# Kernel optimization log

Hardware: AMD Instinct MI355X
Metric: run time of the kernel (lower is better)

## Reference

```python
import jax, jax.numpy as jnp
import numpy as np

B, T, E, DH = 4, 4096, 1024, 128

def setup_inputs() -> dict:
    key = jax.random.key(0)
    k1, k2, k3, k4 = jax.random.split(key, 4)
    scale = 1.0 / np.sqrt(E)
    return {
        "norm_inputs": jax.random.normal(k1, (B, T, E), dtype=jnp.float32),
        "Wq": jax.random.normal(k2, (E, DH), dtype=jnp.float32) * scale,
        "Wk": jax.random.normal(k3, (E, DH), dtype=jnp.float32) * scale,
        "Wv": jax.random.normal(k4, (E, DH), dtype=jnp.float32) * scale,
    }

def reference(norm_inputs, Wq, Wk, Wv):
    # q,k,v: [B,T,DH]
    q = jnp.einsum("bte,ed->btd", norm_inputs, Wq)
    k = jnp.einsum("bte,ed->btd", norm_inputs, Wk)
    v = jnp.einsum("bte,ed->btd", norm_inputs, Wv)
    Tn = norm_inputs.shape[1]
    # scaled scores [B,T,T]
    scores = jnp.einsum("bqd,bkd->bqk", q, k) / jnp.sqrt(jnp.asarray(q.shape[-1], q.dtype))
    causal = jnp.tril(jnp.ones((Tn, Tn), dtype=bool))
    scores = jnp.where(causal, scores, -jnp.inf)
    attn = jax.nn.softmax(scores, axis=-1)  # dropout p=0 -> identity
    return jnp.einsum("bqk,bkd->bqd", attn, v)
```

## Files before the change

### kernel.cpp

```cpp
#include <hip/hip_runtime.h>
#include <hip/hip_bf16.h>

#define NB 4
#define NT 4096
#define NE 1024
#define ND 128
#define QSCALE 0.12751741f

typedef unsigned u32x4 __attribute__((ext_vector_type(4)));
typedef float f32x4 __attribute__((ext_vector_type(4)));
typedef float f32x16 __attribute__((ext_vector_type(16)));
typedef __bf16 bf16x8 __attribute__((ext_vector_type(8)));
typedef unsigned short u16;

__device__ __forceinline__ unsigned cvt_pk_bf16(float lo, float hi) {
  unsigned r;
  asm("v_cvt_pk_bf16_f32 %0, %1, %2" : "=v"(r) : "v"(lo), "v"(hi));
  return r;
}
__device__ __forceinline__ void permswap(unsigned& a, unsigned& b) {
  asm("v_permlane32_swap_b32 %0, %1" : "+v"(a), "+v"(b));
}
__device__ __forceinline__ u16 f2bf(float f) {
  unsigned x = __float_as_uint(f);
  x += 0x7fffu + ((x >> 16) & 1u);
  return (u16)(x >> 16);
}
__device__ __forceinline__ float bf2f(u16 u) {
  return __uint_as_float(((unsigned)u) << 16);
}
__device__ __forceinline__ f32x16 mfma32(bf16x8 a, bf16x8 b, f32x16 c) {
  return __builtin_amdgcn_mfma_f32_32x32x16_bf16(a, b, c, 0, 0, 0);
}
__device__ __forceinline__ bf16x8 ldb(const u16* p) {
  return *reinterpret_cast<const bf16x8*>(p);
}
__device__ __forceinline__ void pack_pf(const f32x16& pr, bf16x8& f0, bf16x8& f1) {
  unsigned pk[8];
#pragma unroll
  for (int i = 0; i < 8; ++i) pk[i] = cvt_pk_bf16(pr[2 * i], pr[2 * i + 1]);
  permswap(pk[0], pk[2]);
  permswap(pk[1], pk[3]);
  permswap(pk[4], pk[6]);
  permswap(pk[5], pk[7]);
  u32x4 t0, t1;
  t0[0] = pk[0]; t0[1] = pk[1]; t0[2] = pk[2]; t0[3] = pk[3];
  t1[0] = pk[4]; t1[1] = pk[5]; t1[2] = pk[6]; t1[3] = pk[7];
  f0 = __builtin_bit_cast(bf16x8, t0);
  f1 = __builtin_bit_cast(bf16x8, t1);
}

__global__ void ah_prep(const float* __restrict__ Wq, const float* __restrict__ Wk,
                        const float* __restrict__ Wv, u16* __restrict__ wt) {
  const int m = blockIdx.x >> 5;
  const int r = blockIdx.x & 31;
  const int e0 = (r >> 1) * 64;
  const int d0 = (r & 1) * 64;
  const float* W = (m == 0) ? Wq : (m == 1) ? Wk : Wv;
  const float s = (m == 0) ? QSCALE : 1.0f;
  __shared__ u16 lds[64][68];
  const int t = threadIdx.x;
  const int row = t >> 2;
  const int c0 = (t & 3) * 16;
  const float* src = W + (size_t)(e0 + row) * ND + d0 + c0;
#pragma unroll
  for (int i = 0; i < 16; i += 4) {
    f32x4 v = *reinterpret_cast<const f32x4*>(src + i);
#pragma unroll
    for (int j = 0; j < 4; ++j) lds[c0 + i + j][row] = f2bf(v[j] * s);
  }
  __syncthreads();
  const int d = t >> 2;
  const int ec = (t & 3) * 16;
  u16* dst = wt + (size_t)m * NE * ND + (size_t)(d0 + d) * NE + e0 + ec;
  u32x4 o0, o1;
#pragma unroll
  for (int j = 0; j < 4; ++j)
    o0[j] = (unsigned)lds[d][ec + 2 * j] | ((unsigned)lds[d][ec + 2 * j + 1] << 16);
#pragma unroll
  for (int j = 0; j < 4; ++j)
    o1[j] = (unsigned)lds[d][ec + 8 + 2 * j] | ((unsigned)lds[d][ec + 8 + 2 * j + 1] << 16);
  *reinterpret_cast<u32x4*>(dst) = o0;
  *reinterpret_cast<u32x4*>(dst + 8) = o1;
}

__global__ __launch_bounds__(256, 2) void ah_proj(
    const float* __restrict__ X, const u16* __restrict__ wt,
    u16* __restrict__ qb, u16* __restrict__ kb, u16* __restrict__ vtb) {
  const int row0 = blockIdx.x * 32;
  const int tid = threadIdx.x;
  const int w = tid >> 6;
  const int lane = tid & 63;
  const int l31 = lane & 31;
  const int h = lane >> 5;

  const float* xrow = X + (size_t)(row0 + l31) * NE + h * 8;
  const u16* wpQ = wt + (size_t)(w * 32 + l31) * NE + h * 8;
  const u16* wpK = wpQ + (size_t)NE * ND;
  const u16* wpV = wpK + (size_t)NE * ND;

  f32x16 accQ = {}, accK = {}, accV = {};

#pragma unroll 4
  for (int e0 = 0; e0 < NE; e0 += 16) {
    f32x4 x0 = *reinterpret_cast<const f32x4*>(xrow + e0);
    f32x4 x1 = *reinterpret_cast<const f32x4*>(xrow + e0 + 4);
    u32x4 xw;
    xw[0] = cvt_pk_bf16(x0[0], x0[1]);
    xw[1] = cvt_pk_bf16(x0[2], x0[3]);
    xw[2] = cvt_pk_bf16(x1[0], x1[1]);
    xw[3] = cvt_pk_bf16(x1[2], x1[3]);
    bf16x8 xf = __builtin_bit_cast(bf16x8, xw);
    accQ = mfma32(xf, ldb(wpQ + e0), accQ);
    accK = mfma32(xf, ldb(wpK + e0), accK);
    accV = mfma32(ldb(wpV + e0), xf, accV);
  }

  const int col = w * 32 + l31;
#pragma unroll
  for (int r = 0; r < 16; ++r) {
    const int trow = row0 + (r & 3) + 8 * (r >> 2) + 4 * h;
    qb[(size_t)trow * ND + col] = f2bf(accQ[r]);
    kb[(size_t)trow * ND + col] = f2bf(accK[r]);
  }
  const int bb = row0 >> 12;
  const int tt = (row0 & 4095) + l31;
#pragma unroll
  for (int r = 0; r < 16; ++r) {
    const int d = w * 32 + (r & 3) + 8 * (r >> 2) + 4 * h;
    vtb[(size_t)bb * ND * NT + (size_t)d * NT + tt] = f2bf(accV[r]);
  }
}

__global__ __launch_bounds__(256, 4) void ah_attn_sk(
    const u16* __restrict__ qg, const u16* __restrict__ kg,
    const u16* __restrict__ vtg, u16* __restrict__ opart,
    float* __restrict__ ml) {
  __shared__ float smem_m[4][32];
  __shared__ float smem_l[4][32];
  __shared__ float smemO[128][33];

  const int bid = blockIdx.x;
  const int x = bid & 7;
  const int s = bid >> 3;
  const int b = x >> 1;
  const int p = x & 1;
  int r, c;
  if (s < 64)       { r = s >> 2;               c = s & 3; }
  else if (s < 112) { int t = s - 64; int q3 = t / 3; r = 16 + q3; c = t - 3 * q3; }
  else if (s < 144) { int t = s - 112; r = 32 + (t >> 1); c = t & 1; }
  else              { r = 48 + (s - 144);       c = 0; }
  const int qt = (126 + p) - 2 * r;
  const int q0 = qt * 32;
  const int jbeg = c * 32;
  const int jend = min(jbeg + 32, qt + 1);

  const int tid = threadIdx.x;
  const int w = tid >> 6;
  const int lane = tid & 63;
  const int l31 = lane & 31;
  const int h = lane >> 5;

  const u16* Qb = qg + (size_t)b * NT * ND;
  const u16* Kb = kg + (size_t)b * NT * ND;
  const u16* VTb = vtg + (size_t)b * ND * NT;

  bf16x8 qf[8];
  {
    const u16* qrow = Qb + (size_t)(q0 + l31) * ND + h * 8;
#pragma unroll
    for (int sI = 0; sI < 8; ++sI) qf[sI] = ldb(qrow + sI * 16);
  }

  float m_run = -1e30f, l_run = 0.f;
  f32x16 ot[4] = {};

  for (int j0 = jbeg + w; j0 < jend; j0 += 8) {
    const int j1 = j0 + 4;
    const bool has1 = (j1 < jend);
    const int k0 = j0 * 32;
    const int k1 = has1 ? j1 * 32 : k0;
    f32x16 sa = {}, sb = {};
    const u16* krow0 = Kb + (size_t)(k0 + l31) * ND + h * 8;
    const u16* krow1 = Kb + (size_t)(k1 + l31) * ND + h * 8;
#pragma unroll
    for (int sI = 0; sI < 8; ++sI) {
      sa = mfma32(ldb(krow0 + sI * 16), qf[sI], sa);
      sb = mfma32(ldb(krow1 + sI * 16), qf[sI], sb);
    }
    if (j0 == qt) {
#pragma unroll
      for (int r2 = 0; r2 < 16; ++r2) {
        const int kk = (r2 & 3) + 8 * (r2 >> 2) + 4 * h;
        if (kk > l31) sa[r2] = -1e30f;
      }
    }
    if (has1) {
      if (j1 == qt) {
#pragma unroll
        for (int r2 = 0; r2 < 16; ++r2) {
          const int kk = (r2 & 3) + 8 * (r2 >> 2) + 4 * h;
          if (kk > l31) sb[r2] = -1e30f;
        }
      }
    } else {
#pragma unroll
      for (int r2 = 0; r2 < 16; ++r2) sb[r2] = -1e30f;
    }
    float mt = sa[0];
#pragma unroll
    for (int r2 = 1; r2 < 16; ++r2) mt = fmaxf(mt, sa[r2]);
#pragma unroll
    for (int r2 = 0; r2 < 16; ++r2) mt = fmaxf(mt, sb[r2]);
    mt = fmaxf(mt, __shfl_xor(mt, 32));
    if (__any(mt > m_run + 8.f)) {
      const float mn = fmaxf(m_run, mt);
      const float f = __builtin_amdgcn_exp2f(m_run - mn);
      l_run *= f;
#pragma unroll
      for (int d0 = 0; d0 < 4; ++d0) ot[d0] *= f;
      m_run = mn;
    }
    float ps = 0.f;
#pragma unroll
    for (int r2 = 0; r2 < 16; ++r2) {
      sa[r2] = __builtin_amdgcn_exp2f(sa[r2] - m_run);
      ps += sa[r2];
    }
#pragma unroll
    for (int r2 = 0; r2 < 16; ++r2) {
      sb[r2] = __builtin_amdgcn_exp2f(sb[r2] - m_run);
      ps += sb[r2];
    }
    ps += __shfl_xor(ps, 32);
    l_run += ps;
    bf16x8 pf0a, pf0b, pf1a, pf1b;
    pack_pf(sa, pf0a, pf0b);
    pack_pf(sb, pf1a, pf1b);
#pragma unroll
    for (int d0 = 0; d0 < 4; ++d0) {
      const u16* vrow0 = VTb + (size_t)(d0 * 32 + l31) * NT + k0 + h * 8;
      const u16* vrow1 = VTb + (size_t)(d0 * 32 + l31) * NT + k1 + h * 8;
      ot[d0] = mfma32(ldb(vrow0), pf0a, ot[d0]);
      ot[d0] = mfma32(ldb(vrow0 + 16), pf0b, ot[d0]);
      ot[d0] = mfma32(ldb(vrow1), pf1a, ot[d0]);
      ot[d0] = mfma32(ldb(vrow1 + 16), pf1b, ot[d0]);
    }
  }

  if (h == 0) { smem_m[w][l31] = m_run; smem_l[w][l31] = l_run; }
  __syncthreads();
  float mstar = smem_m[0][l31];
#pragma unroll
  for (int wv = 1; wv < 4; ++wv) mstar = fmaxf(mstar, smem_m[wv][l31]);
  float lstar = 0.f;
#pragma unroll
  for (int wv = 0; wv < 4; ++wv)
    lstar += smem_l[wv][l31] * __builtin_amdgcn_exp2f(smem_m[wv][l31] - mstar);
  const float fw = __builtin_amdgcn_exp2f(m_run - mstar);
  for (int rnd = 0; rnd < 4; ++rnd) {
    if (w == rnd) {
#pragma unroll
      for (int d0 = 0; d0 < 4; ++d0)
#pragma unroll
        for (int r2 = 0; r2 < 16; ++r2) {
          const int d = d0 * 32 + (r2 & 3) + 8 * (r2 >> 2) + 4 * h;
          const float v = ot[d0][r2] * fw;
          if (rnd == 0) smemO[d][l31] = v;
          else smemO[d][l31] += v;
        }
    }
    __syncthreads();
  }
  const int slot = ((b * 128 + qt) << 2) + c;
  if (tid < 32) {
    ml[(size_t)slot * 64 + tid] = mstar;
    ml[(size_t)slot * 64 + 32 + tid] = lstar;
  }
  {
    const int q = tid >> 3;
    const int dbase = (tid & 7) * 16;
    u32x4 o0, o1;
#pragma unroll
    for (int k = 0; k < 4; ++k)
      o0[k] = cvt_pk_bf16(smemO[dbase + 2 * k][q], smemO[dbase + 2 * k + 1][q]);
#pragma unroll
    for (int k = 0; k < 4; ++k)
      o1[k] = cvt_pk_bf16(smemO[dbase + 8 + 2 * k][q], smemO[dbase + 9 + 2 * k][q]);
    u16* dst = opart + (size_t)slot * 4096 + q * ND + dbase;
    *reinterpret_cast<u32x4*>(dst) = o0;
    *reinterpret_cast<u32x4*>(dst + 8) = o1;
  }
}

__global__ __launch_bounds__(256, 4) void ah_comb(
    const u16* __restrict__ opart, const float* __restrict__ ml,
    float* __restrict__ out) {
  const int bid = blockIdx.x;
  const int x = bid & 7;
  const int r = bid >> 3;
  const int b = x >> 1;
  const int p = x & 1;
  const int qt = (126 + p) - 2 * r;
  const int q0 = qt * 32;
  const int nch = (qt + 32) >> 5;
  const int slot0 = (b * 128 + qt) << 2;

  const int tid = threadIdx.x;
  const int q = tid >> 3;
  const int dbase = (tid & 7) * 16;

  float mi0 = -1e30f, mi1 = -1e30f, mi2 = -1e30f, mi3 = -1e30f;
  mi0 = ml[(size_t)slot0 * 64 + q];
  if (nch > 1) mi1 = ml[(size_t)(slot0 + 1) * 64 + q];
  if (nch > 2) mi2 = ml[(size_t)(slot0 + 2) * 64 + q];
  if (nch > 3) mi3 = ml[(size_t)(slot0 + 3) * 64 + q];
  const float M = fmaxf(fmaxf(mi0, mi1), fmaxf(mi2, mi3));
  float sc0 = __builtin_amdgcn_exp2f(mi0 - M);
  float sc1 = __builtin_amdgcn_exp2f(mi1 - M);
  float sc2 = __builtin_amdgcn_exp2f(mi2 - M);
  float sc3 = __builtin_amdgcn_exp2f(mi3 - M);
  float L = ml[(size_t)slot0 * 64 + 32 + q] * sc0;
  if (nch > 1) L += ml[(size_t)(slot0 + 1) * 64 + 32 + q] * sc1;
  if (nch > 2) L += ml[(size_t)(slot0 + 2) * 64 + 32 + q] * sc2;
  if (nch > 3) L += ml[(size_t)(slot0 + 3) * 64 + 32 + q] * sc3;

  float acc[16];
#pragma unroll
  for (int k = 0; k < 16; ++k) acc[k] = 0.f;
#pragma unroll
  for (int i = 0; i < 4; ++i) {
    if (i < nch) {
      const float sc = (i == 0) ? sc0 : (i == 1) ? sc1 : (i == 2) ? sc2 : sc3;
      const u16* src = opart + (size_t)(slot0 + i) * 4096 + q * ND + dbase;
      u32x4 w0 = *reinterpret_cast<const u32x4*>(src);
      u32x4 w1 = *reinterpret_cast<const u32x4*>(src + 8);
#pragma unroll
      for (int k = 0; k < 4; ++k) {
        acc[2 * k] += sc * __uint_as_float(w0[k] << 16);
        acc[2 * k + 1] += sc * __uint_as_float(w0[k] & 0xffff0000u);
        acc[8 + 2 * k] += sc * __uint_as_float(w1[k] << 16);
        acc[9 + 2 * k] += sc * __uint_as_float(w1[k] & 0xffff0000u);
      }
    }
  }
  const float linv = 1.0f / L;
  float* orow = out + (size_t)b * NT * ND + (size_t)(q0 + q) * ND + dbase;
#pragma unroll
  for (int cc = 0; cc < 4; ++cc) {
    f32x4 v4;
#pragma unroll
    for (int e = 0; e < 4; ++e) v4[e] = acc[cc * 4 + e] * linv;
    *reinterpret_cast<f32x4*>(orow + cc * 4) = v4;
  }
}

extern "C" void kernel_launch(void* const* d_in, const int* in_sizes, int n_in,
                              void* d_out, int out_size, void* d_ws, size_t ws_size,
                              hipStream_t stream) {
  const float* X = (const float*)d_in[0];
  const float* Wq = (const float*)d_in[1];
  const float* Wk = (const float*)d_in[2];
  const float* Wv = (const float*)d_in[3];
  u16* ws = (u16*)d_ws;
  u16* wt = ws;
  u16* qb = wt + 393216;
  u16* kb = qb + 2097152;
  u16* vtb = kb + 2097152;
  u16* opart = vtb + 2097152;
  float* ml = (float*)(opart + 8388608);
  float* out = (float*)d_out;

  ah_prep<<<96, 256, 0, stream>>>(Wq, Wk, Wv, wt);
  ah_proj<<<512, 256, 0, stream>>>(X, wt, qb, kb, vtb);
  ah_attn_sk<<<1280, 256, 0, stream>>>(qb, kb, vtb, opart, ml);
  ah_comb<<<512, 256, 0, stream>>>(opart, ml, out);
}
```

Before: 312.0 us.

## Rebalance split-K attention: split only long query tiles, write short ones directly

The projection kernel now launches one block per (row tile, matrix), three times as many blocks, each with a single accumulator, and uses XCD-aware row mapping. Attention now splits only the 64 longest query tiles per batch into two halves. Shorter tiles are processed whole, normalized and written straight to the output, so the combine kernel only merges two partials for the long tiles. This cuts partial-output traffic and combine work and evens out per-block work. In exchange, each X row is read three times in the projection kernel, and attention occupancy drops to 2 blocks per CU.

```diff
diff --git a/kernel.cpp b/kernel.cpp
--- a/kernel.cpp
+++ b/kernel.cpp
@@ -25,9 +25,6 @@
   unsigned x = __float_as_uint(f);
   x += 0x7fffu + ((x >> 16) & 1u);
   return (u16)(x >> 16);
-}
-__device__ __forceinline__ float bf2f(u16 u) {
-  return __uint_as_float(((unsigned)u) << 16);
 }
 __device__ __forceinline__ f32x16 mfma32(bf16x8 a, bf16x8 b, f32x16 c) {
   return __builtin_amdgcn_mfma_f32_32x32x16_bf16(a, b, c, 0, 0, 0);
@@ -87,7 +84,11 @@
 __global__ __launch_bounds__(256, 2) void ah_proj(
     const float* __restrict__ X, const u16* __restrict__ wt,
     u16* __restrict__ qb, u16* __restrict__ kb, u16* __restrict__ vtb) {
-  const int row0 = blockIdx.x * 32;
+  const int x = blockIdx.x & 7;
+  const int s = blockIdx.x >> 3;
+  const int rtl = s / 3;
+  const int mat = s - 3 * rtl;
+  const int row0 = (x * 64 + rtl) * 32;
   const int tid = threadIdx.x;
   const int w = tid >> 6;
   const int lane = tid & 63;
@@ -95,65 +96,88 @@
   const int h = lane >> 5;
 
   const float* xrow = X + (size_t)(row0 + l31) * NE + h * 8;
-  const u16* wpQ = wt + (size_t)(w * 32 + l31) * NE + h * 8;
-  const u16* wpK = wpQ + (size_t)NE * ND;
-  const u16* wpV = wpK + (size_t)NE * ND;
-
-  f32x16 accQ = {}, accK = {}, accV = {};
-
+  const u16* wp = wt + (size_t)mat * NE * ND + (size_t)(w * 32 + l31) * NE + h * 8;
+
+  f32x16 acc = {};
+
+  if (mat < 2) {
 #pragma unroll 4
-  for (int e0 = 0; e0 < NE; e0 += 16) {
-    f32x4 x0 = *reinterpret_cast<const f32x4*>(xrow + e0);
-    f32x4 x1 = *reinterpret_cast<const f32x4*>(xrow + e0 + 4);
-    u32x4 xw;
-    xw[0] = cvt_pk_bf16(x0[0], x0[1]);
-    xw[1] = cvt_pk_bf16(x0[2], x0[3]);
-    xw[2] = cvt_pk_bf16(x1[0], x1[1]);
-    xw[3] = cvt_pk_bf16(x1[2], x1[3]);
-    bf16x8 xf = __builtin_bit_cast(bf16x8, xw);
-    accQ = mfma32(xf, ldb(wpQ + e0), accQ);
-    accK = mfma32(xf, ldb(wpK + e0), accK);
-    accV = mfma32(ldb(wpV + e0), xf, accV);
-  }
-
-  const int col = w * 32 + l31;
-#pragma unroll
-  for (int r = 0; r < 16; ++r) {
-    const int trow = row0 + (r & 3) + 8 * (r >> 2) + 4 * h;
-    qb[(size_t)trow * ND + col] = f2bf(accQ[r]);
-    kb[(size_t)trow * ND + col] = f2bf(accK[r]);
-  }
-  const int bb = row0 >> 12;
-  const int tt = (row0 & 4095) + l31;
-#pragma unroll
-  for (int r = 0; r < 16; ++r) {
-    const int d = w * 32 + (r & 3) + 8 * (r >> 2) + 4 * h;
-    vtb[(size_t)bb * ND * NT + (size_t)d * NT + tt] = f2bf(accV[r]);
-  }
-}
-
-__global__ __launch_bounds__(256, 4) void ah_attn_sk(
+    for (int e0 = 0; e0 < NE; e0 += 16) {
+      f32x4 x0 = *reinterpret_cast<const f32x4*>(xrow + e0);
+      f32x4 x1 = *reinterpret_cast<const f32x4*>(xrow + e0 + 4);
+      u32x4 xw;
+      xw[0] = cvt_pk_bf16(x0[0], x0[1]);
+      xw[1] = cvt_pk_bf16(x0[2], x0[3]);
+      xw[2] = cvt_pk_bf16(x1[0], x1[1]);
+      xw[3] = cvt_pk_bf16(x1[2], x1[3]);
+      bf16x8 xf = __builtin_bit_cast(bf16x8, xw);
+      acc = mfma32(xf, ldb(wp + e0), acc);
+    }
+    u16* dst = (mat == 0) ? qb : kb;
+    const int col = w * 32 + l31;
+#pragma unroll
+    for (int r = 0; r < 16; ++r) {
+      const int trow = row0 + (r & 3) + 8 * (r >> 2) + 4 * h;
+      dst[(size_t)trow * ND + col] = f2bf(acc[r]);
+    }
+  } else {
+#pragma unroll 4
+    for (int e0 = 0; e0 < NE; e0 += 16) {
+      f32x4 x0 = *reinterpret_cast<const f32x4*>(xrow + e0);
+      f32x4 x1 = *reinterpret_cast<const f32x4*>(xrow + e0 + 4);
+      u32x4 xw;
+      xw[0] = cvt_pk_bf16(x0[0], x0[1]);
+      xw[1] = cvt_pk_bf16(x0[2], x0[3]);
+      xw[2] = cvt_pk_bf16(x1[0], x1[1]);
+      xw[3] = cvt_pk_bf16(x1[2], x1[3]);
+      bf16x8 xf = __builtin_bit_cast(bf16x8, xw);
+      acc = mfma32(ldb(wp + e0), xf, acc);
+    }
+    const int bb = row0 >> 12;
+    const int tt = (row0 & 4095) + l31;
+#pragma unroll
+    for (int r = 0; r < 16; ++r) {
+      const int d = w * 32 + (r & 3) + 8 * (r >> 2) + 4 * h;
+      vtb[(size_t)bb * ND * NT + (size_t)d * NT + tt] = f2bf(acc[r]);
+    }
+  }
+}
+
+__global__ __launch_bounds__(256, 2) void ah_attn(
     const u16* __restrict__ qg, const u16* __restrict__ kg,
     const u16* __restrict__ vtg, u16* __restrict__ opart,
-    float* __restrict__ ml) {
+    float* __restrict__ ml, float* __restrict__ out) {
   __shared__ float smem_m[4][32];
   __shared__ float smem_l[4][32];
+  __shared__ float smem_linv[32];
   __shared__ float smemO[128][33];
 
   const int bid = blockIdx.x;
   const int x = bid & 7;
-  const int s = bid >> 3;
+  const int sh = bid >> 3;
   const int b = x >> 1;
-  const int p = x & 1;
-  int r, c;
-  if (s < 64)       { r = s >> 2;               c = s & 3; }
-  else if (s < 112) { int t = s - 64; int q3 = t / 3; r = 16 + q3; c = t - 3 * q3; }
-  else if (s < 144) { int t = s - 112; r = 32 + (t >> 1); c = t & 1; }
-  else              { r = 48 + (s - 144);       c = 0; }
-  const int qt = (126 + p) - 2 * r;
+  const int s = sh * 2 + (x & 1);
+  int qt, c, jbeg, jend, split;
+  {
+    const int q3 = s / 3;
+    const int rem = s - 3 * q3;
+    if (rem < 2) {
+      const int i = q3 * 2 + rem;
+      qt = 127 - (i >> 1);
+      c = i & 1;
+      const int n0 = (qt + 2) >> 1;
+      split = 1;
+      jbeg = c ? n0 : 0;
+      jend = c ? (qt + 1) : n0;
+    } else {
+      qt = 63 - q3;
+      c = 0;
+      split = 0;
+      jbeg = 0;
+      jend = qt + 1;
+    }
+  }
   const int q0 = qt * 32;
-  const int jbeg = c * 32;
-  const int jend = min(jbeg + 32, qt + 1);
 
   const int tid = threadIdx.x;
   const int w = tid >> 6;
@@ -257,6 +281,7 @@
 #pragma unroll
   for (int wv = 0; wv < 4; ++wv)
     lstar += smem_l[wv][l31] * __builtin_amdgcn_exp2f(smem_m[wv][l31] - mstar);
+  if (!split && tid < 32) smem_linv[tid] = 1.0f / lstar;
   const float fw = __builtin_amdgcn_exp2f(m_run - mstar);
   for (int rnd = 0; rnd < 4; ++rnd) {
     if (w == rnd) {
@@ -272,14 +297,24 @@
     }
     __syncthreads();
   }
-  const int slot = ((b * 128 + qt) << 2) + c;
-  if (tid < 32) {
-    ml[(size_t)slot * 64 + tid] = mstar;
-    ml[(size_t)slot * 64 + 32 + tid] = lstar;
-  }
-  {
-    const int q = tid >> 3;
-    const int dbase = (tid & 7) * 16;
+  const int q = tid >> 3;
+  const int dbase = (tid & 7) * 16;
+  if (!split) {
+    const float linv = smem_linv[q];
+    float* orow = out + (size_t)b * NT * ND + (size_t)(q0 + q) * ND + dbase;
+#pragma unroll
+    for (int cc = 0; cc < 4; ++cc) {
+      f32x4 v4;
+#pragma unroll
+      for (int e = 0; e < 4; ++e) v4[e] = smemO[dbase + cc * 4 + e][q] * linv;
+      *reinterpret_cast<f32x4*>(orow + cc * 4) = v4;
+    }
+  } else {
+    const int slot = ((b << 6) + (qt - 64)) * 2 + c;
+    if (tid < 32) {
+      ml[(size_t)slot * 64 + tid] = mstar;
+      ml[(size_t)slot * 64 + 32 + tid] = lstar;
+    }
     u32x4 o0, o1;
 #pragma unroll
     for (int k = 0; k < 4; ++k)
@@ -297,54 +332,38 @@
     const u16* __restrict__ opart, const float* __restrict__ ml,
     float* __restrict__ out) {
   const int bid = blockIdx.x;
-  const int x = bid & 7;
-  const int r = bid >> 3;
-  const int b = x >> 1;
-  const int p = x & 1;
-  const int qt = (126 + p) - 2 * r;
+  const int b = bid >> 6;
+  const int qt = 64 + (bid & 63);
   const int q0 = qt * 32;
-  const int nch = (qt + 32) >> 5;
-  const int slot0 = (b * 128 + qt) << 2;
+  const int slot0 = ((b << 6) + (qt - 64)) * 2;
 
   const int tid = threadIdx.x;
   const int q = tid >> 3;
   const int dbase = (tid & 7) * 16;
 
-  float mi0 = -1e30f, mi1 = -1e30f, mi2 = -1e30f, mi3 = -1e30f;
-  mi0 = ml[(size_t)slot0 * 64 + q];
-  if (nch > 1) mi1 = ml[(size_t)(slot0 + 1) * 64 + q];
-  if (nch > 2) mi2 = ml[(size_t)(slot0 + 2) * 64 + q];
-  if (nch > 3) mi3 = ml[(size_t)(slot0 + 3) * 64 + q];
-  const float M = fmaxf(fmaxf(mi0, mi1), fmaxf(mi2, mi3));
-  float sc0 = __builtin_amdgcn_exp2f(mi0 - M);
-  float sc1 = __builtin_amdgcn_exp2f(mi1 - M);
-  float sc2 = __builtin_amdgcn_exp2f(mi2 - M);
-  float sc3 = __builtin_amdgcn_exp2f(mi3 - M);
-  float L = ml[(size_t)slot0 * 64 + 32 + q] * sc0;
-  if (nch > 1) L += ml[(size_t)(slot0 + 1) * 64 + 32 + q] * sc1;
-  if (nch > 2) L += ml[(size_t)(slot0 + 2) * 64 + 32 + q] * sc2;
-  if (nch > 3) L += ml[(size_t)(slot0 + 3) * 64 + 32 + q] * sc3;
-
+  const float m0 = ml[(size_t)slot0 * 64 + q];
+  const float m1 = ml[(size_t)(slot0 + 1) * 64 + q];
+  const float M = fmaxf(m0, m1);
+  const float sc0 = __builtin_amdgcn_exp2f(m0 - M);
+  const float sc1 = __builtin_amdgcn_exp2f(m1 - M);
+  const float L = ml[(size_t)slot0 * 64 + 32 + q] * sc0 +
+                  ml[(size_t)(slot0 + 1) * 64 + 32 + q] * sc1;
+  const float linv = 1.0f / L;
+
+  const u16* s0 = opart + (size_t)slot0 * 4096 + q * ND + dbase;
+  const u16* s1 = s0 + 4096;
+  u32x4 a0 = *reinterpret_cast<const u32x4*>(s0);
+  u32x4 a1 = *reinterpret_cast<const u32x4*>(s0 + 8);
+  u32x4 b0 = *reinterpret_cast<const u32x4*>(s1);
+  u32x4 b1 = *reinterpret_cast<const u32x4*>(s1 + 8);
   float acc[16];
 #pragma unroll
-  for (int k = 0; k < 16; ++k) acc[k] = 0.f;
-#pragma unroll
-  for (int i = 0; i < 4; ++i) {
-    if (i < nch) {
-      const float sc = (i == 0) ? sc0 : (i == 1) ? sc1 : (i == 2) ? sc2 : sc3;
-      const u16* src = opart + (size_t)(slot0 + i) * 4096 + q * ND + dbase;
-      u32x4 w0 = *reinterpret_cast<const u32x4*>(src);
-      u32x4 w1 = *reinterpret_cast<const u32x4*>(src + 8);
-#pragma unroll
-      for (int k = 0; k < 4; ++k) {
-        acc[2 * k] += sc * __uint_as_float(w0[k] << 16);
-        acc[2 * k + 1] += sc * __uint_as_float(w0[k] & 0xffff0000u);
-        acc[8 + 2 * k] += sc * __uint_as_float(w1[k] << 16);
-        acc[9 + 2 * k] += sc * __uint_as_float(w1[k] & 0xffff0000u);
-      }
-    }
-  }
-  const float linv = 1.0f / L;
+  for (int k = 0; k < 4; ++k) {
+    acc[2 * k]     = sc0 * __uint_as_float(a0[k] << 16) + sc1 * __uint_as_float(b0[k] << 16);
+    acc[2 * k + 1] = sc0 * __uint_as_float(a0[k] & 0xffff0000u) + sc1 * __uint_as_float(b0[k] & 0xffff0000u);
+    acc[8 + 2 * k] = sc0 * __uint_as_float(a1[k] << 16) + sc1 * __uint_as_float(b1[k] << 16);
+    acc[9 + 2 * k] = sc0 * __uint_as_float(a1[k] & 0xffff0000u) + sc1 * __uint_as_float(b1[k] & 0xffff0000u);
+  }
   float* orow = out + (size_t)b * NT * ND + (size_t)(q0 + q) * ND + dbase;
 #pragma unroll
   for (int cc = 0; cc < 4; ++cc) {
@@ -368,11 +387,11 @@
   u16* kb = qb + 2097152;
   u16* vtb = kb + 2097152;
   u16* opart = vtb + 2097152;
-  float* ml = (float*)(opart + 8388608);
+  float* ml = (float*)(opart + 2097152);
   float* out = (float*)d_out;
 
   ah_prep<<<96, 256, 0, stream>>>(Wq, Wk, Wv, wt);
-  ah_proj<<<512, 256, 0, stream>>>(X, wt, qb, kb, vtb);
-  ah_attn_sk<<<1280, 256, 0, stream>>>(qb, kb, vtb, opart, ml);
-  ah_comb<<<512, 256, 0, stream>>>(opart, ml, out);
-}
+  ah_proj<<<1536, 256, 0, stream>>>(X, wt, qb, kb, vtb);
+  ah_attn<<<768, 256, 0, stream>>>(qb, kb, vtb, opart, ml, out);
+  ah_comb<<<256, 256, 0, stream>>>(opart, ml, out);
+}
```

New measurement: 311.7 us. About the same (-0.1%).
